# Performance work log

Measured on AMD Instinct MI355X. Metric: run time of the kernel, lower is better.

## Reference

```python
import jax, jax.numpy as jnp
import numpy as np

PRUNE_RATIO = 0.5
NOISE_SCALE = 0.1
MIXUP_ALPHA = 0.05
TEMPERATURE = 0.5
B, N, D = 32, 4096, 256


def setup_inputs() -> dict:
    key = jax.random.key(0)
    k1, k2, k3 = jax.random.split(key, 3)
    seq = jax.random.normal(k1, (B, N, D), dtype=jnp.float32)
    attn_weights = jax.random.uniform(k2, (B, N), dtype=jnp.float32)
    uniform_noise = jax.random.uniform(k3, (B, N), dtype=jnp.float32)
    return {"seq": seq, "attn_weights": attn_weights, "uniform_noise": uniform_noise}


def reference(seq, attn_weights, uniform_noise):
    b, n, d = seq.shape
    k = max(1, int(n * (1.0 - PRUNE_RATIO)))
    # training branch: gumbel noise from the provided uniform draw
    gumbel = -jnp.log(-jnp.log(uniform_noise + 1e-10) + 1e-10)
    noisy = attn_weights + NOISE_SCALE * gumbel                      # (B, N)
    soft = jax.nn.softmax(noisy / TEMPERATURE, axis=-1)              # (B, N)
    _, top_idx = jax.lax.top_k(soft, k)                              # (B, K) int32
    # gather selected tokens: (B, K, D)
    selected = jnp.take_along_axis(seq, top_idx[:, :, None], axis=1)
    # mixup: mean of the pruned (non-selected) tokens
    mask = jnp.ones((b, n), dtype=seq.dtype).at[
        jnp.arange(b)[:, None], top_idx
    ].set(0.0)                                                       # (B, N), 1 on pruned
    remaining_sum = jnp.einsum('bn,bnd->bd', mask, seq)              # (B, D)
    remaining_count = mask.sum(axis=1, keepdims=True) + 1e-10        # (B, 1)
    remaining_mean = remaining_sum / remaining_count                 # (B, D)
    return selected + MIXUP_ALPHA * remaining_mean[:, None, :]       # (B, K, D)
```

## Files before the change

kernel.cpp:

```cpp
#include <hip/hip_runtime.h>
#include <hip/hip_bf16.h>

#define B_ 32
#define N_ 4096
#define D_ 256
#define K_ 2048

__global__ __launch_bounds__(256) void key_kernel(
    const float* __restrict__ attn, const float* __restrict__ noise,
    unsigned long long* __restrict__ keys, float* __restrict__ meanAccum) {
  const int t = blockIdx.x * 256 + threadIdx.x;
  float u = noise[t];
  float a = attn[t];
  float x = __fadd_rn(u, 1e-10f);
  float l1 = (float)log((double)x);
  float inner = __fadd_rn(-l1, 1e-10f);
  float g = -(float)log((double)inner);
  float noisy = __fadd_rn(a, __fmul_rn(0.1f, g));
  unsigned int fb = __float_as_uint(noisy);
  fb = (fb & 0x80000000u) ? ~fb : (fb | 0x80000000u);
  int i = t & (N_ - 1);
  keys[t] = ((unsigned long long)fb << 32) | (unsigned int)(~i);
  if (t < B_ * D_) meanAccum[t] = 0.0f;
}

__global__ __launch_bounds__(256) void rank_kernel(
    const unsigned long long* __restrict__ keys, int* __restrict__ sortedIdx) {
  __shared__ __align__(16) unsigned long long lk[N_];
  const int b = blockIdx.y;

  const ulonglong2* gk = (const ulonglong2*)(keys + (size_t)b * N_);
  ulonglong2* lk2 = (ulonglong2*)lk;
  for (int i = threadIdx.x; i < N_ / 2; i += 256) lk2[i] = gk[i];
  __syncthreads();

  const int i = blockIdx.x * 256 + threadIdx.x;
  const unsigned long long ki = lk[i];
  int rank = 0;
#pragma unroll 8
  for (int j = 0; j < N_ / 2; ++j) {
    ulonglong2 v = lk2[j];
    rank += (v.x > ki);
    rank += (v.y > ki);
  }
  sortedIdx[(size_t)b * N_ + rank] = i;
}

__global__ __launch_bounds__(256) void mean_kernel(
    const float* __restrict__ seq, const int* __restrict__ sortedIdx,
    float* __restrict__ meanAccum) {
  const int b = blockIdx.y;
  const int chunk = blockIdx.x;
  const int tid = threadIdx.x;
  const int dv = tid & 63;
  const int sub = tid >> 6;
  const int base = b * N_ + K_ + chunk * 128;

  float4 acc = make_float4(0.f, 0.f, 0.f, 0.f);
  for (int r = sub; r < 128; r += 4) {
    int idx = sortedIdx[base + r];
    const float4* row = (const float4*)(seq + ((size_t)b * N_ + idx) * D_);
    float4 v = row[dv];
    acc.x += v.x; acc.y += v.y; acc.z += v.z; acc.w += v.w;
  }

  __shared__ float4 red[4][64];
  red[sub][dv] = acc;
  __syncthreads();
  if (sub == 0) {
    float4 s0 = red[0][dv], s1 = red[1][dv], s2 = red[2][dv], s3 = red[3][dv];
    float sx = s0.x + s1.x + s2.x + s3.x;
    float sy = s0.y + s1.y + s2.y + s3.y;
    float sz = s0.z + s1.z + s2.z + s3.z;
    float sw = s0.w + s1.w + s2.w + s3.w;
    float* dst = meanAccum + b * D_ + dv * 4;
    atomicAdd(dst + 0, sx);
    atomicAdd(dst + 1, sy);
    atomicAdd(dst + 2, sz);
    atomicAdd(dst + 3, sw);
  }
}

__global__ __launch_bounds__(256) void out_kernel(
    const float* __restrict__ seq, const int* __restrict__ sortedIdx,
    const float* __restrict__ meanAccum, float* __restrict__ out) {
  const unsigned int t = blockIdx.x * 256u + threadIdx.x;
  const int dv = t & 63;
  const int j = (t >> 6) & (K_ - 1);
  const int b = t >> 17;

  int idx = sortedIdx[b * N_ + j];
  float4 v = ((const float4*)(seq + ((size_t)b * N_ + idx) * D_))[dv];
  float4 m = ((const float4*)(meanAccum + b * D_))[dv];
  const float inv_cnt = 1.0f / 2048.0f;
  float4 o;
  o.x = v.x + 0.05f * (m.x * inv_cnt);
  o.y = v.y + 0.05f * (m.y * inv_cnt);
  o.z = v.z + 0.05f * (m.z * inv_cnt);
  o.w = v.w + 0.05f * (m.w * inv_cnt);
  ((float4*)out)[t] = o;
}

extern "C" void kernel_launch(void* const* d_in, const int* in_sizes, int n_in,
                              void* d_out, int out_size, void* d_ws, size_t ws_size,
                              hipStream_t stream) {
  const float* seq  = (const float*)d_in[0];
  const float* attn = (const float*)d_in[1];
  const float* nois = (const float*)d_in[2];
  float* out = (float*)d_out;

  int* sortedIdx   = (int*)d_ws;
  float* meanAccum = (float*)((char*)d_ws + (size_t)B_ * N_ * 4);
  unsigned long long* keys =
      (unsigned long long*)((char*)d_ws + (size_t)B_ * N_ * 4 + (size_t)B_ * D_ * 4);

  key_kernel<<<(B_ * N_) / 256, 256, 0, stream>>>(attn, nois, keys, meanAccum);
  rank_kernel<<<dim3(N_ / 256, B_), 256, 0, stream>>>(keys, sortedIdx);
  mean_kernel<<<dim3(16, B_), 256, 0, stream>>>(seq, sortedIdx, meanAccum);
  const int total4 = B_ * K_ * (D_ / 4);
  out_kernel<<<total4 / 256, 256, 0, stream>>>(seq, sortedIdx, meanAccum, out);
}
```

Baseline: 293.6 us.

## Fuse rank and pruned-mean kernels, read keys directly from global memory

Merges the ranking kernel and the mean-accumulation kernel so each ranking block collects its pruned tokens in shared memory and sums their rows immediately, removing a launch and the dependency on the sorted index array for the mean. The rank loop now reads keys directly from global memory with wide uniform loads instead of staging them in LDS first. This trades LDS broadcast reads for cached uniform global loads and gives an uneven number of rows to sum per block.

Result: slower. 313.6 us (+6.8%).

```diff
diff --git a/kernel.cpp b/kernel.cpp
--- a/kernel.cpp
+++ b/kernel.cpp
@@ -1,5 +1,4 @@
 #include <hip/hip_runtime.h>
-#include <hip/hip_bf16.h>
 
 #define B_ 32
 #define N_ 4096
@@ -24,42 +23,42 @@
   if (t < B_ * D_) meanAccum[t] = 0.0f;
 }
 
-__global__ __launch_bounds__(256) void rank_kernel(
-    const unsigned long long* __restrict__ keys, int* __restrict__ sortedIdx) {
-  __shared__ __align__(16) unsigned long long lk[N_];
+__global__ __launch_bounds__(256) void rank_mean_kernel(
+    const unsigned long long* __restrict__ keys, const float* __restrict__ seq,
+    int* __restrict__ sortedIdx, float* __restrict__ meanAccum) {
   const int b = blockIdx.y;
+  const int i = blockIdx.x * 256 + threadIdx.x;
+  const unsigned long long* __restrict__ bk = keys + (size_t)b * N_;
+  const unsigned long long ki = bk[i];
 
-  const ulonglong2* gk = (const ulonglong2*)(keys + (size_t)b * N_);
-  ulonglong2* lk2 = (ulonglong2*)lk;
-  for (int i = threadIdx.x; i < N_ / 2; i += 256) lk2[i] = gk[i];
-  __syncthreads();
-
-  const int i = blockIdx.x * 256 + threadIdx.x;
-  const unsigned long long ki = lk[i];
   int rank = 0;
-#pragma unroll 8
-  for (int j = 0; j < N_ / 2; ++j) {
-    ulonglong2 v = lk2[j];
+  const ulonglong4* __restrict__ bk4 = (const ulonglong4*)bk;
+#pragma unroll 4
+  for (int j = 0; j < N_ / 4; ++j) {
+    ulonglong4 v = bk4[j];
     rank += (v.x > ki);
     rank += (v.y > ki);
+    rank += (v.z > ki);
+    rank += (v.w > ki);
   }
   sortedIdx[(size_t)b * N_ + rank] = i;
-}
 
-__global__ __launch_bounds__(256) void mean_kernel(
-    const float* __restrict__ seq, const int* __restrict__ sortedIdx,
-    float* __restrict__ meanAccum) {
-  const int b = blockIdx.y;
-  const int chunk = blockIdx.x;
-  const int tid = threadIdx.x;
-  const int dv = tid & 63;
-  const int sub = tid >> 6;
-  const int base = b * N_ + K_ + chunk * 128;
+  __shared__ int plist[256];
+  __shared__ int pcount;
+  if (threadIdx.x == 0) pcount = 0;
+  __syncthreads();
+  if (rank >= K_) {
+    int slot = atomicAdd(&pcount, 1);
+    plist[slot] = i;
+  }
+  __syncthreads();
+  const int cnt = pcount;
 
+  const int dv = threadIdx.x & 63;
+  const int sub = threadIdx.x >> 6;
   float4 acc = make_float4(0.f, 0.f, 0.f, 0.f);
-  for (int r = sub; r < 128; r += 4) {
-    int idx = sortedIdx[base + r];
-    const float4* row = (const float4*)(seq + ((size_t)b * N_ + idx) * D_);
+  for (int r = sub; r < cnt; r += 4) {
+    const float4* row = (const float4*)(seq + ((size_t)b * N_ + plist[r]) * D_);
     float4 v = row[dv];
     acc.x += v.x; acc.y += v.y; acc.z += v.z; acc.w += v.w;
   }
@@ -115,8 +114,7 @@
       (unsigned long long*)((char*)d_ws + (size_t)B_ * N_ * 4 + (size_t)B_ * D_ * 4);
 
   key_kernel<<<(B_ * N_) / 256, 256, 0, stream>>>(attn, nois, keys, meanAccum);
-  rank_kernel<<<dim3(N_ / 256, B_), 256, 0, stream>>>(keys, sortedIdx);
-  mean_kernel<<<dim3(16, B_), 256, 0, stream>>>(seq, sortedIdx, meanAccum);
+  rank_mean_kernel<<<dim3(N_ / 256, B_), 256, 0, stream>>>(keys, seq, sortedIdx, meanAccum);
   const int total4 = B_ * K_ * (D_ / 4);
   out_kernel<<<total4 / 256, 256, 0, stream>>>(seq, sortedIdx, meanAccum, out);
 }
```
